# Kernel tuning notes

Hardware: AMD Instinct MI355X
Metric: run time of the kernel (lower is better)

## Reference

```python
import jax, jax.numpy as jnp
import numpy as np

H = 1024       # hidden_size
VOCAB = 32000  # output_size
L = 128        # max_length
B = 64         # batch


def setup_inputs() -> dict:
    key = jax.random.key(0)
    ks = jax.random.split(key, 16)
    inp = {
        "input_ids": jax.random.randint(ks[0], (1, B), 0, VOCAB),
        "hidden": jax.random.normal(ks[1], (1, B, H), jnp.float32),
        "encoder_outputs": jax.random.normal(ks[2], (L, B, H), jnp.float32),
        # parameters
        "emb": jax.random.normal(ks[3], (VOCAB, H), jnp.float32) * 0.02,
        "attn_W": jax.random.normal(ks[4], (H, 2 * H), jnp.float32) * 0.02,
        "attn_b": jnp.zeros((H,), jnp.float32),
        "v": jax.random.uniform(ks[5], (H,), jnp.float32),
        "w_ih": jax.random.normal(ks[6], (3 * H, 2 * H), jnp.float32) * 0.02,
        "w_hh": jax.random.normal(ks[7], (3 * H, H), jnp.float32) * 0.02,
        "b_ih": jnp.zeros((3 * H,), jnp.float32),
        "b_hh": jnp.zeros((3 * H,), jnp.float32),
        "out_W": jax.random.normal(ks[8], (VOCAB, 3 * H), jnp.float32) * 0.02,
        "out_b": jnp.zeros((VOCAB,), jnp.float32),
    }
    return inp


def reference(input_ids, hidden, encoder_outputs, emb, attn_W, attn_b, v,
              w_ih, w_hh, b_ih, b_hh, out_W, out_b):
    # Dropout in eval mode (identity).
    embedded = emb[input_ids]                      # [1, B, H]
    eo = jnp.transpose(encoder_outputs, (1, 0, 2))  # [B, L, H]
    h0 = hidden[0]                                  # [B, H]

    # Additive (Bahdanau) attention score
    h_rep = jnp.broadcast_to(h0[:, None, :], (eo.shape[0], eo.shape[1], h0.shape[-1]))
    cat = jnp.concatenate([eo, h_rep], axis=-1)     # [B, L, 2H]
    energy = jnp.tanh(jnp.einsum('blk,hk->blh', cat, attn_W) + attn_b)  # [B, L, H]
    scores = jnp.einsum('blh,h->bl', energy, v)     # [B, L]
    attention = jax.nn.softmax(scores, axis=-1)     # [B, L]
    weighted = jnp.einsum('bl,blh->bh', attention, eo)  # [B, H]

    # GRU cell (single layer, single timestep), PyTorch gate order r,z,n
    x = jnp.concatenate([embedded[0], weighted], axis=-1)  # [B, 2H]
    gx = x @ w_ih.T + b_ih                                  # [B, 3H]
    gh = h0 @ w_hh.T + b_hh                                 # [B, 3H]
    xr, xz, xn = jnp.split(gx, 3, axis=-1)
    hr, hz, hn = jnp.split(gh, 3, axis=-1)
    r = jax.nn.sigmoid(xr + hr)
    z = jax.nn.sigmoid(xz + hz)
    n = jnp.tanh(xn + r * hn)
    h_new = (1.0 - z) * n + z * h0                          # [B, H]

    out_cat = jnp.concatenate([h_new, weighted, embedded[0]], axis=-1)  # [B, 3H]
    output = out_cat @ out_W.T + out_b                      # [B, VOCAB]
    return output, h_new[None], attention[:, None, :]
```

## Files before the change

### kernel.cpp

```cpp
#include <hip/hip_runtime.h>
#include <math.h>

#define Hdim 1024
#define VOC 32000
#define LSEQ 128
#define BSZ 64

typedef __attribute__((ext_vector_type(8))) short bf16x8;
typedef __attribute__((ext_vector_type(4))) float f32x4;

__device__ __forceinline__ float fast_tanhf(float x) {
    return 1.0f - 2.0f / (__expf(2.0f * x) + 1.0f);
}
__device__ __forceinline__ float sigmoidf(float x) {
    return 1.0f / (1.0f + __expf(-x));
}
__device__ __forceinline__ short f2bf(float f) {
    unsigned u = __float_as_uint(f);
    unsigned r = (u + 0x7fffu + ((u >> 16) & 1u)) >> 16;
    return (short)r;
}

__device__ __forceinline__ void gl_lds16(const short* g, short* l) {
    __builtin_amdgcn_global_load_lds(
        (const __attribute__((address_space(1))) unsigned*)g,
        (__attribute__((address_space(3))) unsigned*)l, 16, 0, 0);
}

__device__ __forceinline__ void stage16(const float* __restrict__ src, short* dst) {
    f32x4 v0 = *(const f32x4*)(src);
    f32x4 v1 = *(const f32x4*)(src + 4);
    f32x4 v2 = *(const f32x4*)(src + 8);
    f32x4 v3 = *(const f32x4*)(src + 12);
    bf16x8 p0, p1;
    p0[0] = f2bf(v0[0]); p0[1] = f2bf(v0[1]); p0[2] = f2bf(v0[2]); p0[3] = f2bf(v0[3]);
    p0[4] = f2bf(v1[0]); p0[5] = f2bf(v1[1]); p0[6] = f2bf(v1[2]); p0[7] = f2bf(v1[3]);
    p1[0] = f2bf(v2[0]); p1[1] = f2bf(v2[1]); p1[2] = f2bf(v2[2]); p1[3] = f2bf(v2[3]);
    p1[4] = f2bf(v3[0]); p1[5] = f2bf(v3[1]); p1[6] = f2bf(v3[2]); p1[7] = f2bf(v3[3]);
    *(bf16x8*)(dst) = p0;
    *(bf16x8*)(dst + 8) = p1;
}

__global__ __launch_bounds__(256) void convert_bf16(
    const float* __restrict__ enc, const float* __restrict__ attnW,
    const float* __restrict__ hidden,
    short* __restrict__ enc_bf, short* __restrict__ attnW_bf,
    short* __restrict__ hidden_bf)
{
    const int NG_ENC = (LSEQ * BSZ * Hdim) / 8;
    const int NG_AW  = (Hdim * 2 * Hdim) / 8;
    const int NG_H   = (BSZ * Hdim) / 8;
    const int total = NG_ENC + NG_AW + NG_H;
    for (int g = blockIdx.x * 256 + threadIdx.x; g < total; g += gridDim.x * 256) {
        const float* src; short* dst; int idx;
        if (g < NG_ENC)              { src = enc;    dst = enc_bf;    idx = g; }
        else if (g < NG_ENC + NG_AW) { src = attnW;  dst = attnW_bf;  idx = g - NG_ENC; }
        else                         { src = hidden; dst = hidden_bf; idx = g - NG_ENC - NG_AW; }
        f32x4 a = *(const f32x4*)(src + (size_t)idx * 8);
        f32x4 b = *(const f32x4*)(src + (size_t)idx * 8 + 4);
        bf16x8 p;
        p[0] = f2bf(a[0]); p[1] = f2bf(a[1]); p[2] = f2bf(a[2]); p[3] = f2bf(a[3]);
        p[4] = f2bf(b[0]); p[5] = f2bf(b[1]); p[6] = f2bf(b[2]); p[7] = f2bf(b[3]);
        *(bf16x8*)(dst + (size_t)idx * 8) = p;
    }
}

__global__ __launch_bounds__(256) void ugemm(
    const short* __restrict__ A,
    const short* __restrict__ B,
    float* __restrict__ C)
{
    __shared__ short As[64 * 72];
    __shared__ short Bs[128 * 72];

    const int t = threadIdx.x;
    const int lane = t & 63, wave = t >> 6;
    const int lr = lane & 15, kh = lane >> 4;
    const int n0 = blockIdx.x * 128;
    const int kstart = blockIdx.y * 256;
    float* Cp = C + (size_t)blockIdx.y * (BSZ * Hdim);

    const int ar = t >> 2, ac = (t & 3) * 16;
    const int br = t >> 1, bc = (t & 1) * 32;

    f32x4 acc[4][2] = {};

    for (int k0 = 0; k0 < 256; k0 += 64) {
        const int kg = kstart + k0;
        {
            const short* s = A + (size_t)ar * Hdim + kg + ac;
            *(bf16x8*)(As + ar * 72 + ac)     = *(const bf16x8*)(s);
            *(bf16x8*)(As + ar * 72 + ac + 8) = *(const bf16x8*)(s + 8);
        }
        {
            const short* s = B + (size_t)(n0 + br) * (2 * Hdim) + kg + bc;
            short* d = Bs + br * 72 + bc;
            *(bf16x8*)(d)      = *(const bf16x8*)(s);
            *(bf16x8*)(d + 8)  = *(const bf16x8*)(s + 8);
            *(bf16x8*)(d + 16) = *(const bf16x8*)(s + 16);
            *(bf16x8*)(d + 24) = *(const bf16x8*)(s + 24);
        }
        __syncthreads();
#pragma unroll
        for (int kk = 0; kk < 64; kk += 32) {
            bf16x8 af[4], bfr[2];
#pragma unroll
            for (int mi = 0; mi < 4; ++mi)
                af[mi] = *(const bf16x8*)(As + (mi * 16 + lr) * 72 + kk + kh * 8);
#pragma unroll
            for (int ni = 0; ni < 2; ++ni)
                bfr[ni] = *(const bf16x8*)(Bs + (wave * 32 + ni * 16 + lr) * 72 + kk + kh * 8);
#pragma unroll
            for (int mi = 0; mi < 4; ++mi)
#pragma unroll
                for (int ni = 0; ni < 2; ++ni)
                    acc[mi][ni] = __builtin_amdgcn_mfma_f32_16x16x32_bf16(
                        af[mi], bfr[ni], acc[mi][ni], 0, 0, 0);
        }
        __syncthreads();
    }

#pragma unroll
    for (int mi = 0; mi < 4; ++mi)
#pragma unroll
        for (int ni = 0; ni < 2; ++ni) {
            const int col = n0 + wave * 32 + ni * 16 + lr;
#pragma unroll
            for (int r = 0; r < 4; ++r) {
                const int row = mi * 16 + kh * 4 + r;
                Cp[(size_t)row * Hdim + col] = acc[mi][ni][r];
            }
        }
}

__global__ __launch_bounds__(512) void attn_scores_mfma(
    const short* __restrict__ enc_bf,
    const short* __restrict__ W1_bf,
    const float* __restrict__ u4,
    const float* __restrict__ attnb,
    const float* __restrict__ vvec,
    float* __restrict__ scores_part)
{
    __shared__ short As[128 * 64];
    __shared__ short Bs[128 * 64];
    __shared__ float red[8][64];
    __shared__ float u_lds[64 * 128];

    const int t = threadIdx.x;
    const int lane = t & 63, wave = t >> 6;
    const int wr = wave >> 2, wc = wave & 3;
    const int lr = lane & 15, kh = lane >> 4;
    const int m0 = blockIdx.x * 128;
    const int n0 = blockIdx.y * 128;

    const int o1 = t * 16;
    const int o2 = 8192 + t * 16;
    const int r1 = o1 >> 7, c1 = (o1 & 127) >> 1;
    const int r2 = o2 >> 7, c2 = (o2 & 127) >> 1;

    for (int i = t; i < 64 * 128; i += 512) {
        const int b = i >> 7, hl = i & 127;
        const size_t g = (size_t)b * Hdim + n0 + hl;
        u_lds[i] = u4[g] + u4[65536 + g] + u4[2 * 65536 + g] + u4[3 * 65536 + g]
                 + attnb[n0 + hl];
    }

    f32x4 acc[4][2] = {};

    for (int kg = 0; kg < Hdim; kg += 64) {
        gl_lds16(enc_bf + (size_t)(m0 + r1) * Hdim + kg + c1, As + (o1 >> 1));
        gl_lds16(enc_bf + (size_t)(m0 + r2) * Hdim + kg + c2, As + (o2 >> 1));
        gl_lds16(W1_bf + (size_t)(n0 + r1) * (2 * Hdim) + kg + c1, Bs + (o1 >> 1));
        gl_lds16(W1_bf + (size_t)(n0 + r2) * (2 * Hdim) + kg + c2, Bs + (o2 >> 1));
        __syncthreads();
#pragma unroll
        for (int kk = 0; kk < 64; kk += 32) {
            bf16x8 af[4], bfr[2];
#pragma unroll
            for (int mi = 0; mi < 4; ++mi)
                af[mi] = *(const bf16x8*)(As + (wr * 64 + mi * 16 + lr) * 64 + kk + kh * 8);
#pragma unroll
            for (int ni = 0; ni < 2; ++ni)
                bfr[ni] = *(const bf16x8*)(Bs + (wc * 32 + ni * 16 + lr) * 64 + kk + kh * 8);
#pragma unroll
            for (int mi = 0; mi < 4; ++mi)
#pragma unroll
                for (int ni = 0; ni < 2; ++ni)
                    acc[mi][ni] = __builtin_amdgcn_mfma_f32_16x16x32_bf16(
                        af[mi], bfr[ni], acc[mi][ni], 0, 0, 0);
        }
        __syncthreads();
    }

    float sv[16];
#pragma unroll
    for (int mi = 0; mi < 4; ++mi)
#pragma unroll
        for (int r = 0; r < 4; ++r) {
            const int lrow = mi * 16 + kh * 4 + r;
            const int b = lrow;
            float s = 0.0f;
#pragma unroll
            for (int ni = 0; ni < 2; ++ni) {
                const int hl = wc * 32 + ni * 16 + lr;
                const float e = fast_tanhf(acc[mi][ni][r] + u_lds[b * 128 + hl]);
                s += e * vvec[n0 + hl];
            }
            sv[mi * 4 + r] = s;
        }
#pragma unroll
    for (int i = 0; i < 16; ++i) {
#pragma unroll
        for (int d = 1; d < 16; d <<= 1)
            sv[i] += __shfl_xor(sv[i], d, 64);
    }
    if (lr == 0) {
#pragma unroll
        for (int mi = 0; mi < 4; ++mi)
#pragma unroll
            for (int r = 0; r < 4; ++r)
                red[wave][mi * 16 + kh * 4 + r] = sv[mi * 4 + r];
    }
    __syncthreads();
    if (t < 128) {
        const int wrr = t >> 6, lrow = t & 63;
        scores_part[(size_t)blockIdx.y * (LSEQ * BSZ) + m0 + t] =
            red[wrr * 4 + 0][lrow] + red[wrr * 4 + 1][lrow] +
            red[wrr * 4 + 2][lrow] + red[wrr * 4 + 3][lrow];
    }
}

__global__ __launch_bounds__(128) void softmax_weighted(
    const float* __restrict__ sp,
    const short* __restrict__ enc_bf,
    const int* __restrict__ ids,
    const float* __restrict__ emb,
    float* __restrict__ attn_out,
    short* __restrict__ x_bf,
    short* __restrict__ oc_bf)
{
    const int b = blockIdx.x, hg = blockIdx.y, t = threadIdx.x;
    __shared__ float aw[LSEQ];
    __shared__ float red[LSEQ];

    if (hg == 0) {
        const int id = ids[b];
        const int h = t * 8;
        f32x4 e0 = *(const f32x4*)(emb + (size_t)id * Hdim + h);
        f32x4 e1 = *(const f32x4*)(emb + (size_t)id * Hdim + h + 4);
        bf16x8 p;
        p[0] = f2bf(e0[0]); p[1] = f2bf(e0[1]); p[2] = f2bf(e0[2]); p[3] = f2bf(e0[3]);
        p[4] = f2bf(e1[0]); p[5] = f2bf(e1[1]); p[6] = f2bf(e1[2]); p[7] = f2bf(e1[3]);
        *(bf16x8*)(x_bf + (size_t)b * 2048 + h) = p;
        *(bf16x8*)(oc_bf + (size_t)b * 3072 + 2048 + h) = p;
    }

    float s = 0.0f;
#pragma unroll
    for (int g = 0; g < 8; ++g) s += sp[g * (LSEQ * BSZ) + t * 64 + b];
    red[t] = s;
    __syncthreads();
    for (int off = 64; off > 0; off >>= 1) {
        if (t < off) red[t] = fmaxf(red[t], red[t + off]);
        __syncthreads();
    }
    const float mx = red[0];
    __syncthreads();
    const float e = __expf(s - mx);
    red[t] = e;
    __syncthreads();
    for (int off = 64; off > 0; off >>= 1) {
        if (t < off) red[t] += red[t + off];
        __syncthreads();
    }
    const float p = e / red[0];
    aw[t] = p;
    if (hg == 0) attn_out[(size_t)b * LSEQ + t] = p;
    __syncthreads();

    const int h = hg * 256 + t * 2;
    float a0 = 0.0f, a1 = 0.0f;
#pragma unroll 8
    for (int l = 0; l < LSEQ; ++l) {
        const unsigned w = *(const unsigned*)(enc_bf + ((size_t)l * BSZ + b) * Hdim + h);
        const float pw = aw[l];
        a0 = fmaf(pw, __uint_as_float(w << 16), a0);
        a1 = fmaf(pw, __uint_as_float(w & 0xffff0000u), a1);
    }
    const unsigned packed = (unsigned)(unsigned short)f2bf(a0)
                          | ((unsigned)(unsigned short)f2bf(a1) << 16);
    *(unsigned*)(x_bf + (size_t)b * 2048 + 1024 + h) = packed;
    *(unsigned*)(oc_bf + (size_t)b * 3072 + 1024 + h) = packed;
}

__device__ __forceinline__ void sgemm_body(
    const short* __restrict__ A, int lda,
    const float* __restrict__ B, int ldb,
    const float* __restrict__ bias,
    float* __restrict__ C, int ldc,
    int n0, int kstart, int klen)
{
    __shared__ short As[2][64 * 72];
    __shared__ short Bs[2][64 * 72];

    const int t = threadIdx.x;
    const int lane = t & 63, wave = t >> 6;
    const int wm = wave >> 2, wn = wave & 3;
    const int lr = lane & 15, kh = lane >> 4;

    const int sr = t >> 3, sc = (t & 7) * 8;
    const short* Ap = A + (size_t)sr * lda + kstart + sc;
    const float* Bp = B + (size_t)(n0 + sr) * ldb + kstart + sc;

    const int nkt = klen >> 6;

    bf16x8 pa = *(const bf16x8*)(Ap);
    f32x4 pb0 = *(const f32x4*)(Bp);
    f32x4 pb1 = *(const f32x4*)(Bp + 4);
    *(bf16x8*)(&As[0][sr * 72 + sc]) = pa;
    {
        bf16x8 q;
        q[0] = f2bf(pb0[0]); q[1] = f2bf(pb0[1]); q[2] = f2bf(pb0[2]); q[3] = f2bf(pb0[3]);
        q[4] = f2bf(pb1[0]); q[5] = f2bf(pb1[1]); q[6] = f2bf(pb1[2]); q[7] = f2bf(pb1[3]);
        *(bf16x8*)(&Bs[0][sr * 72 + sc]) = q;
    }

    f32x4 acc[2] = {};

    for (int kt = 0; kt < nkt; ++kt) {
        const int cur = kt & 1;
        if (kt + 1 < nkt) {
            const int kn = (kt + 1) * 64;
            pa  = *(const bf16x8*)(Ap + kn);
            pb0 = *(const f32x4*)(Bp + kn);
            pb1 = *(const f32x4*)(Bp + kn + 4);
        }
        __syncthreads();
#pragma unroll
        for (int kk = 0; kk < 64; kk += 32) {
            bf16x8 af0 = *(const bf16x8*)(&As[cur][(wm * 32 + lr) * 72 + kk + kh * 8]);
            bf16x8 af1 = *(const bf16x8*)(&As[cur][(wm * 32 + 16 + lr) * 72 + kk + kh * 8]);
            bf16x8 bfr = *(const bf16x8*)(&Bs[cur][(wn * 16 + lr) * 72 + kk + kh * 8]);
            acc[0] = __builtin_amdgcn_mfma_f32_16x16x32_bf16(af0, bfr, acc[0], 0, 0, 0);
            acc[1] = __builtin_amdgcn_mfma_f32_16x16x32_bf16(af1, bfr, acc[1], 0, 0, 0);
        }
        if (kt + 1 < nkt) {
            const int nxt = cur ^ 1;
            *(bf16x8*)(&As[nxt][sr * 72 + sc]) = pa;
            bf16x8 q;
            q[0] = f2bf(pb0[0]); q[1] = f2bf(pb0[1]); q[2] = f2bf(pb0[2]); q[3] = f2bf(pb0[3]);
            q[4] = f2bf(pb1[0]); q[5] = f2bf(pb1[1]); q[6] = f2bf(pb1[2]); q[7] = f2bf(pb1[3]);
            *(bf16x8*)(&Bs[nxt][sr * 72 + sc]) = q;
        }
    }

    const int col = n0 + wn * 16 + lr;
    const float bb = bias ? bias[col] : 0.0f;
#pragma unroll
    for (int mi = 0; mi < 2; ++mi)
#pragma unroll
        for (int r = 0; r < 4; ++r) {
            const int row = wm * 32 + mi * 16 + kh * 4 + r;
            C[(size_t)row * ldc + col] = acc[mi][r] + bb;
        }
}

__global__ __launch_bounds__(512) void outproj_stream(
    const short* __restrict__ A, const float* __restrict__ B,
    const float* __restrict__ bias, float* __restrict__ logits)
{
    sgemm_body(A, 3 * Hdim, B, 3 * Hdim, bias, logits, VOC,
               blockIdx.x * 64, 0, 3 * Hdim);
}

__global__ __launch_bounds__(512) void gxgh_stream(
    const short* __restrict__ x_bf, const float* __restrict__ w_ih,
    const short* __restrict__ hidden_bf, const float* __restrict__ w_hh,
    float* __restrict__ gx4, float* __restrict__ gh4)
{
    const size_t P = (size_t)BSZ * 3 * Hdim;
    if (blockIdx.x < 48)
        sgemm_body(x_bf, 2 * Hdim, w_ih, 2 * Hdim, nullptr,
                   gx4 + blockIdx.y * P, 3 * Hdim,
                   blockIdx.x * 64, blockIdx.y * 512, 512);
    else
        sgemm_body(hidden_bf, Hdim, w_hh, Hdim, nullptr,
                   gh4 + blockIdx.y * P, 3 * Hdim,
                   (blockIdx.x - 48) * 64, blockIdx.y * 256, 256);
}

__global__ __launch_bounds__(256) void gru_kernel(
    const float* __restrict__ gx4, const float* __restrict__ gh4,
    const float* __restrict__ b_ih, const float* __restrict__ b_hh,
    const float* __restrict__ h0,
    float* __restrict__ hnew_out, short* __restrict__ oc_bf)
{
    const int idx = blockIdx.x * 256 + threadIdx.x;
    const int b = idx >> 10, h = idx & 1023;
    const size_t g3 = (size_t)b * (3 * Hdim);
    const size_t P = (size_t)BSZ * 3 * Hdim;
    float xr = b_ih[h], xz = b_ih[Hdim + h], xn = b_ih[2 * Hdim + h];
    float hr = b_hh[h], hz = b_hh[Hdim + h], hn = b_hh[2 * Hdim + h];
#pragma unroll
    for (int s = 0; s < 4; ++s) {
        xr += gx4[s * P + g3 + h];
        xz += gx4[s * P + g3 + Hdim + h];
        xn += gx4[s * P + g3 + 2 * Hdim + h];
        hr += gh4[s * P + g3 + h];
        hz += gh4[s * P + g3 + Hdim + h];
        hn += gh4[s * P + g3 + 2 * Hdim + h];
    }
    const float r = sigmoidf(xr + hr);
    const float z = sigmoidf(xz + hz);
    const float n = fast_tanhf(xn + r * hn);
    const float hv = (1.0f - z) * n + z * h0[(size_t)b * Hdim + h];
    hnew_out[(size_t)b * Hdim + h] = hv;
    oc_bf[g3 + h] = f2bf(hv);
}

extern "C" void kernel_launch(void* const* d_in, const int* in_sizes, int n_in,
                              void* d_out, int out_size, void* d_ws, size_t ws_size,
                              hipStream_t stream)
{
    const int*   ids    = (const int*)d_in[0];
    const float* hidden = (const float*)d_in[1];
    const float* enc    = (const float*)d_in[2];
    const float* emb    = (const float*)d_in[3];
    const float* attnW  = (const float*)d_in[4];
    const float* attnb  = (const float*)d_in[5];
    const float* vvec   = (const float*)d_in[6];
    const float* w_ih   = (const float*)d_in[7];
    const float* w_hh   = (const float*)d_in[8];
    const float* b_ih   = (const float*)d_in[9];
    const float* b_hh   = (const float*)d_in[10];
    const float* out_W  = (const float*)d_in[11];
    const float* out_b  = (const float*)d_in[12];

    float* out        = (float*)d_out;
    float* out_logits = out;
    float* out_hnew   = out + (size_t)BSZ * VOC;
    float* out_attn   = out_hnew + (size_t)BSZ * Hdim;

    float* ws = (float*)d_ws;
    short* enc_bf    = (short*)ws;
    short* attnW_bf  = (short*)(ws + 4194304);
    short* hidden_bf = (short*)(ws + 5242880);
    float* ws_u4  = ws + 5275648;
    float* ws_sp  = ws_u4 + 262144;
    short* x_bf   = (short*)(ws_sp + 65536);
    short* oc_bf  = (short*)(ws_sp + 131072);
    float* ws_gx4 = ws_sp + 229376;
    float* ws_gh4 = ws_gx4 + 786432;

    convert_bf16<<<dim3(1024), 256, 0, stream>>>(
        enc, attnW, hidden, enc_bf, attnW_bf, hidden_bf);

    ugemm<<<dim3(Hdim / 128, 4), 256, 0, stream>>>(
        hidden_bf, attnW_bf + Hdim, ws_u4);

    attn_scores_mfma<<<dim3(LSEQ / 2, 8), 512, 0, stream>>>(
        enc_bf, attnW_bf, ws_u4, attnb, vvec, ws_sp);

    softmax_weighted<<<dim3(BSZ, 4), 128, 0, stream>>>(
        ws_sp, enc_bf, ids, emb, out_attn, x_bf, oc_bf);

    gxgh_stream<<<dim3(96, 4), 512, 0, stream>>>(
        x_bf, w_ih, hidden_bf, w_hh, ws_gx4, ws_gh4);

    gru_kernel<<<dim3(BSZ * Hdim / 256), 256, 0, stream>>>(
        ws_gx4, ws_gh4, b_ih, b_hh, hidden, out_hnew, oc_bf);

    outproj_stream<<<dim3(VOC / 64), 512, 0, stream>>>(
        oc_bf, out_W, out_b, out_logits);
}
```

Before: 174.1 us.

## Split output projection and overlap embedding part with attention GEMM

The output projection is split by K. The embedding slice of out_W, which only needs the embedding, now runs in the same launch as the attention-score GEMM, with blocks interleaved. The remaining h_new/weighted slice runs last and accumulates into the logits. The bf16 conversion and the hidden·W2 u-GEMM are fused into one launch that also gathers the embedding, and only the needed half of attn_W is converted. This removes launches and fills idle CUs during the attention phase, at the cost of a second read-modify-write pass over the logits and more complex block dispatch.

```diff
diff --git a/kernel.cpp b/kernel.cpp
--- a/kernel.cpp
+++ b/kernel.cpp
@@ -41,45 +41,54 @@
     *(bf16x8*)(dst + 8) = p1;
 }
 
-__global__ __launch_bounds__(256) void convert_bf16(
+__global__ __launch_bounds__(256) void conv_ug(
     const float* __restrict__ enc, const float* __restrict__ attnW,
-    const float* __restrict__ hidden,
-    short* __restrict__ enc_bf, short* __restrict__ attnW_bf,
-    short* __restrict__ hidden_bf)
-{
-    const int NG_ENC = (LSEQ * BSZ * Hdim) / 8;
-    const int NG_AW  = (Hdim * 2 * Hdim) / 8;
-    const int NG_H   = (BSZ * Hdim) / 8;
-    const int total = NG_ENC + NG_AW + NG_H;
-    for (int g = blockIdx.x * 256 + threadIdx.x; g < total; g += gridDim.x * 256) {
-        const float* src; short* dst; int idx;
-        if (g < NG_ENC)              { src = enc;    dst = enc_bf;    idx = g; }
-        else if (g < NG_ENC + NG_AW) { src = attnW;  dst = attnW_bf;  idx = g - NG_ENC; }
-        else                         { src = hidden; dst = hidden_bf; idx = g - NG_ENC - NG_AW; }
-        f32x4 a = *(const f32x4*)(src + (size_t)idx * 8);
-        f32x4 b = *(const f32x4*)(src + (size_t)idx * 8 + 4);
-        bf16x8 p;
-        p[0] = f2bf(a[0]); p[1] = f2bf(a[1]); p[2] = f2bf(a[2]); p[3] = f2bf(a[3]);
-        p[4] = f2bf(b[0]); p[5] = f2bf(b[1]); p[6] = f2bf(b[2]); p[7] = f2bf(b[3]);
-        *(bf16x8*)(dst + (size_t)idx * 8) = p;
-    }
-}
-
-__global__ __launch_bounds__(256) void ugemm(
-    const short* __restrict__ A,
-    const short* __restrict__ B,
-    float* __restrict__ C)
+    const float* __restrict__ hidden, const float* __restrict__ emb,
+    const int* __restrict__ ids,
+    short* __restrict__ enc_bf, short* __restrict__ attnW1_bf,
+    short* __restrict__ hidden_bf, short* __restrict__ x_bf,
+    float* __restrict__ u4)
 {
     __shared__ short As[64 * 72];
     __shared__ short Bs[128 * 72];
+
+    if (blockIdx.x < 1024) {
+        const int NG_ENC = 1048576, NG_AW = 131072, NG_H = 8192, NG_EMB = 8192;
+        const int total = NG_ENC + NG_AW + NG_H + NG_EMB;
+        for (int g = blockIdx.x * 256 + threadIdx.x; g < total; g += 1024 * 256) {
+            const float* src; short* dst;
+            if (g < NG_ENC) {
+                src = enc + (size_t)g * 8; dst = enc_bf + (size_t)g * 8;
+            } else if (g < NG_ENC + NG_AW) {
+                const int i = g - NG_ENC, h = i >> 7, c = i & 127;
+                src = attnW + (size_t)h * 2048 + c * 8;
+                dst = attnW1_bf + (size_t)h * 1024 + c * 8;
+            } else if (g < NG_ENC + NG_AW + NG_H) {
+                const int i = g - NG_ENC - NG_AW;
+                src = hidden + (size_t)i * 8; dst = hidden_bf + (size_t)i * 8;
+            } else {
+                const int i = g - NG_ENC - NG_AW - NG_H, b = i >> 7, c = i & 127;
+                src = emb + (size_t)ids[b] * Hdim + c * 8;
+                dst = x_bf + (size_t)b * 2048 + c * 8;
+            }
+            f32x4 a = *(const f32x4*)(src);
+            f32x4 b = *(const f32x4*)(src + 4);
+            bf16x8 p;
+            p[0] = f2bf(a[0]); p[1] = f2bf(a[1]); p[2] = f2bf(a[2]); p[3] = f2bf(a[3]);
+            p[4] = f2bf(b[0]); p[5] = f2bf(b[1]); p[6] = f2bf(b[2]); p[7] = f2bf(b[3]);
+            *(bf16x8*)(dst) = p;
+        }
+        return;
+    }
+
+    const int id = blockIdx.x - 1024;
+    const int n0 = (id & 7) * 128;
+    const int kstart = (id >> 3) * 256;
+    float* Cp = u4 + (size_t)(id >> 3) * (BSZ * Hdim);
 
     const int t = threadIdx.x;
     const int lane = t & 63, wave = t >> 6;
     const int lr = lane & 15, kh = lane >> 4;
-    const int n0 = blockIdx.x * 128;
-    const int kstart = blockIdx.y * 256;
-    float* Cp = C + (size_t)blockIdx.y * (BSZ * Hdim);
-
     const int ar = t >> 2, ac = (t & 3) * 16;
     const int br = t >> 1, bc = (t & 1) * 32;
 
@@ -87,19 +96,9 @@
 
     for (int k0 = 0; k0 < 256; k0 += 64) {
         const int kg = kstart + k0;
-        {
-            const short* s = A + (size_t)ar * Hdim + kg + ac;
-            *(bf16x8*)(As + ar * 72 + ac)     = *(const bf16x8*)(s);
-            *(bf16x8*)(As + ar * 72 + ac + 8) = *(const bf16x8*)(s + 8);
-        }
-        {
-            const short* s = B + (size_t)(n0 + br) * (2 * Hdim) + kg + bc;
-            short* d = Bs + br * 72 + bc;
-            *(bf16x8*)(d)      = *(const bf16x8*)(s);
-            *(bf16x8*)(d + 8)  = *(const bf16x8*)(s + 8);
-            *(bf16x8*)(d + 16) = *(const bf16x8*)(s + 16);
-            *(bf16x8*)(d + 24) = *(const bf16x8*)(s + 24);
-        }
+        stage16(hidden + (size_t)ar * Hdim + kg + ac, As + ar * 72 + ac);
+        stage16(attnW + (size_t)(n0 + br) * 2048 + 1024 + kg + bc,      Bs + br * 72 + bc);
+        stage16(attnW + (size_t)(n0 + br) * 2048 + 1024 + kg + bc + 16, Bs + br * 72 + bc + 16);
         __syncthreads();
 #pragma unroll
         for (int kk = 0; kk < 64; kk += 32) {
@@ -126,79 +125,150 @@
         for (int ni = 0; ni < 2; ++ni) {
             const int col = n0 + wave * 32 + ni * 16 + lr;
 #pragma unroll
-            for (int r = 0; r < 4; ++r) {
-                const int row = mi * 16 + kh * 4 + r;
-                Cp[(size_t)row * Hdim + col] = acc[mi][ni][r];
-            }
-        }
-}
-
-__global__ __launch_bounds__(512) void attn_scores_mfma(
-    const short* __restrict__ enc_bf,
-    const short* __restrict__ W1_bf,
-    const float* __restrict__ u4,
-    const float* __restrict__ attnb,
-    const float* __restrict__ vvec,
-    float* __restrict__ scores_part)
-{
-    __shared__ short As[128 * 64];
-    __shared__ short Bs[128 * 64];
-    __shared__ float red[8][64];
-    __shared__ float u_lds[64 * 128];
+            for (int r = 0; r < 4; ++r)
+                Cp[(size_t)(mi * 16 + kh * 4 + r) * Hdim + col] = acc[mi][ni][r];
+        }
+}
+
+__device__ __forceinline__ void sgemm_body(
+    char* smem,
+    const short* __restrict__ A, int lda,
+    const float* __restrict__ B, int ldb,
+    const float* __restrict__ bias,
+    float* __restrict__ C, int ldc,
+    int n0, int kstart, int klen, bool rmw)
+{
+    short* As = (short*)smem;
+    short* Bs = (short*)(smem + 18432);
+
+    const int t = threadIdx.x;
+    const int lane = t & 63, wave = t >> 6;
+    const int wm = wave >> 2, wn = wave & 3;
+    const int lr = lane & 15, kh = lane >> 4;
+
+    const int sr = t >> 3, sc = (t & 7) * 8;
+    const short* Ap = A + (size_t)sr * lda + kstart + sc;
+    const float* Bp = B + (size_t)(n0 + sr) * ldb + kstart + sc;
+
+    const int nkt = klen >> 6;
+
+    bf16x8 pa = *(const bf16x8*)(Ap);
+    f32x4 pb0 = *(const f32x4*)(Bp);
+    f32x4 pb1 = *(const f32x4*)(Bp + 4);
+    *(bf16x8*)(&As[sr * 72 + sc]) = pa;
+    {
+        bf16x8 q;
+        q[0] = f2bf(pb0[0]); q[1] = f2bf(pb0[1]); q[2] = f2bf(pb0[2]); q[3] = f2bf(pb0[3]);
+        q[4] = f2bf(pb1[0]); q[5] = f2bf(pb1[1]); q[6] = f2bf(pb1[2]); q[7] = f2bf(pb1[3]);
+        *(bf16x8*)(&Bs[sr * 72 + sc]) = q;
+    }
+
+    f32x4 acc[2] = {};
+
+    for (int kt = 0; kt < nkt; ++kt) {
+        const int co = (kt & 1) * 4608;
+        if (kt + 1 < nkt) {
+            const int kn = (kt + 1) * 64;
+            pa  = *(const bf16x8*)(Ap + kn);
+            pb0 = *(const f32x4*)(Bp + kn);
+            pb1 = *(const f32x4*)(Bp + kn + 4);
+        }
+        __syncthreads();
+#pragma unroll
+        for (int kk = 0; kk < 64; kk += 32) {
+            bf16x8 af0 = *(const bf16x8*)(&As[co + (wm * 32 + lr) * 72 + kk + kh * 8]);
+            bf16x8 af1 = *(const bf16x8*)(&As[co + (wm * 32 + 16 + lr) * 72 + kk + kh * 8]);
+            bf16x8 bfr = *(const bf16x8*)(&Bs[co + (wn * 16 + lr) * 72 + kk + kh * 8]);
+            acc[0] = __builtin_amdgcn_mfma_f32_16x16x32_bf16(af0, bfr, acc[0], 0, 0, 0);
+            acc[1] = __builtin_amdgcn_mfma_f32_16x16x32_bf16(af1, bfr, acc[1], 0, 0, 0);
+        }
+        if (kt + 1 < nkt) {
+            const int no = ((kt + 1) & 1) * 4608;
+            *(bf16x8*)(&As[no + sr * 72 + sc]) = pa;
+            bf16x8 q;
+            q[0] = f2bf(pb0[0]); q[1] = f2bf(pb0[1]); q[2] = f2bf(pb0[2]); q[3] = f2bf(pb0[3]);
+            q[4] = f2bf(pb1[0]); q[5] = f2bf(pb1[1]); q[6] = f2bf(pb1[2]); q[7] = f2bf(pb1[3]);
+            *(bf16x8*)(&Bs[no + sr * 72 + sc]) = q;
+        }
+    }
+
+    const int col = n0 + wn * 16 + lr;
+    const float bb = bias ? bias[col] : 0.0f;
+#pragma unroll
+    for (int mi = 0; mi < 2; ++mi)
+#pragma unroll
+        for (int r = 0; r < 4; ++r) {
+            const size_t idx = (size_t)(wm * 32 + mi * 16 + kh * 4 + r) * ldc + col;
+            const float prev = rmw ? C[idx] : 0.0f;
+            C[idx] = prev + acc[mi][r] + bb;
+        }
+}
+
+__device__ __forceinline__ void attn_body(
+    char* smem,
+    const short* __restrict__ enc_bf, const short* __restrict__ W1_bf,
+    const float* __restrict__ u4, const float* __restrict__ attnb,
+    const float* __restrict__ vvec, float* __restrict__ scores_part,
+    int aid)
+{
+    short* As = (short*)smem;
+    short* Bs = (short*)(smem + 16384);
+    float* red = (float*)(smem + 32768);
 
     const int t = threadIdx.x;
     const int lane = t & 63, wave = t >> 6;
     const int wr = wave >> 2, wc = wave & 3;
     const int lr = lane & 15, kh = lane >> 4;
-    const int m0 = blockIdx.x * 128;
-    const int n0 = blockIdx.y * 128;
+    const int m0 = (aid & 63) * 128;
+    const int n0 = (aid >> 6) * 128;
 
     const int o1 = t * 16;
     const int o2 = 8192 + t * 16;
     const int r1 = o1 >> 7, c1 = (o1 & 127) >> 1;
     const int r2 = o2 >> 7, c2 = (o2 & 127) >> 1;
 
+    f32x4 acc[4][2] = {};
+
+    for (int kg = 0; kg < Hdim; kg += 64) {
+        gl_lds16(enc_bf + (size_t)(m0 + r1) * Hdim + kg + c1, As + (o1 >> 1));
+        gl_lds16(enc_bf + (size_t)(m0 + r2) * Hdim + kg + c2, As + (o2 >> 1));
+        gl_lds16(W1_bf + (size_t)(n0 + r1) * Hdim + kg + c1, Bs + (o1 >> 1));
+        gl_lds16(W1_bf + (size_t)(n0 + r2) * Hdim + kg + c2, Bs + (o2 >> 1));
+        __syncthreads();
+#pragma unroll
+        for (int kk = 0; kk < 64; kk += 32) {
+            bf16x8 af[4], bfr[2];
+#pragma unroll
+            for (int mi = 0; mi < 4; ++mi)
+                af[mi] = *(const bf16x8*)(As + (wr * 64 + mi * 16 + lr) * 64 + kk + kh * 8);
+#pragma unroll
+            for (int ni = 0; ni < 2; ++ni)
+                bfr[ni] = *(const bf16x8*)(Bs + (wc * 32 + ni * 16 + lr) * 64 + kk + kh * 8);
+#pragma unroll
+            for (int mi = 0; mi < 4; ++mi)
+#pragma unroll
+                for (int ni = 0; ni < 2; ++ni)
+                    acc[mi][ni] = __builtin_amdgcn_mfma_f32_16x16x32_bf16(
+                        af[mi], bfr[ni], acc[mi][ni], 0, 0, 0);
+        }
+        __syncthreads();
+    }
+
+    float* u_lds = (float*)smem;
     for (int i = t; i < 64 * 128; i += 512) {
         const int b = i >> 7, hl = i & 127;
         const size_t g = (size_t)b * Hdim + n0 + hl;
         u_lds[i] = u4[g] + u4[65536 + g] + u4[2 * 65536 + g] + u4[3 * 65536 + g]
                  + attnb[n0 + hl];
     }
-
-    f32x4 acc[4][2] = {};
-
-    for (int kg = 0; kg < Hdim; kg += 64) {
-        gl_lds16(enc_bf + (size_t)(m0 + r1) * Hdim + kg + c1, As + (o1 >> 1));
-        gl_lds16(enc_bf + (size_t)(m0 + r2) * Hdim + kg + c2, As + (o2 >> 1));
-        gl_lds16(W1_bf + (size_t)(n0 + r1) * (2 * Hdim) + kg + c1, Bs + (o1 >> 1));
-        gl_lds16(W1_bf + (size_t)(n0 + r2) * (2 * Hdim) + kg + c2, Bs + (o2 >> 1));
-        __syncthreads();
-#pragma unroll
-        for (int kk = 0; kk < 64; kk += 32) {
-            bf16x8 af[4], bfr[2];
-#pragma unroll
-            for (int mi = 0; mi < 4; ++mi)
-                af[mi] = *(const bf16x8*)(As + (wr * 64 + mi * 16 + lr) * 64 + kk + kh * 8);
-#pragma unroll
-            for (int ni = 0; ni < 2; ++ni)
-                bfr[ni] = *(const bf16x8*)(Bs + (wc * 32 + ni * 16 + lr) * 64 + kk + kh * 8);
-#pragma unroll
-            for (int mi = 0; mi < 4; ++mi)
-#pragma unroll
-                for (int ni = 0; ni < 2; ++ni)
-                    acc[mi][ni] = __builtin_amdgcn_mfma_f32_16x16x32_bf16(
-                        af[mi], bfr[ni], acc[mi][ni], 0, 0, 0);
-        }
-        __syncthreads();
-    }
+    __syncthreads();
 
     float sv[16];
 #pragma unroll
     for (int mi = 0; mi < 4; ++mi)
 #pragma unroll
         for (int r = 0; r < 4; ++r) {
-            const int lrow = mi * 16 + kh * 4 + r;
-            const int b = lrow;
+            const int b = mi * 16 + kh * 4 + r;
             float s = 0.0f;
 #pragma unroll
             for (int ni = 0; ni < 2; ++ni) {
@@ -219,41 +289,48 @@
         for (int mi = 0; mi < 4; ++mi)
 #pragma unroll
             for (int r = 0; r < 4; ++r)
-                red[wave][mi * 16 + kh * 4 + r] = sv[mi * 4 + r];
+                red[wave * 64 + mi * 16 + kh * 4 + r] = sv[mi * 4 + r];
     }
     __syncthreads();
     if (t < 128) {
         const int wrr = t >> 6, lrow = t & 63;
-        scores_part[(size_t)blockIdx.y * (LSEQ * BSZ) + m0 + t] =
-            red[wrr * 4 + 0][lrow] + red[wrr * 4 + 1][lrow] +
-            red[wrr * 4 + 2][lrow] + red[wrr * 4 + 3][lrow];
+        scores_part[(size_t)(aid >> 6) * (LSEQ * BSZ) + m0 + t] =
+            red[(wrr * 4 + 0) * 64 + lrow] + red[(wrr * 4 + 1) * 64 + lrow] +
+            red[(wrr * 4 + 2) * 64 + lrow] + red[(wrr * 4 + 3) * 64 + lrow];
+    }
+}
+
+__global__ __launch_bounds__(512) void attn_oproj(
+    const short* __restrict__ enc_bf, const short* __restrict__ W1_bf,
+    const float* __restrict__ u4, const float* __restrict__ attnb,
+    const float* __restrict__ vvec, float* __restrict__ scores_part,
+    const short* __restrict__ x_bf, const float* __restrict__ out_W,
+    const float* __restrict__ out_b, float* __restrict__ logits)
+{
+    __shared__ __align__(16) char smem[36864];
+    const int i = blockIdx.x;
+    if (i < 1000) {
+        if ((i & 1) == 0)
+            attn_body(smem, enc_bf, W1_bf, u4, attnb, vvec, scores_part, i >> 1);
+        else
+            sgemm_body(smem, x_bf, 2048, out_W + 2048, 3072, out_b,
+                       logits, VOC, (i >> 1) * 64, 0, 1024, false);
+    } else {
+        attn_body(smem, enc_bf, W1_bf, u4, attnb, vvec, scores_part,
+                  500 + (i - 1000));
     }
 }
 
 __global__ __launch_bounds__(128) void softmax_weighted(
     const float* __restrict__ sp,
     const short* __restrict__ enc_bf,
-    const int* __restrict__ ids,
-    const float* __restrict__ emb,
     float* __restrict__ attn_out,
     short* __restrict__ x_bf,
-    short* __restrict__ oc_bf)
+    short* __restrict__ hw_bf)
 {
     const int b = blockIdx.x, hg = blockIdx.y, t = threadIdx.x;
     __shared__ float aw[LSEQ];
     __shared__ float red[LSEQ];
-
-    if (hg == 0) {
-        const int id = ids[b];
-        const int h = t * 8;
-        f32x4 e0 = *(const f32x4*)(emb + (size_t)id * Hdim + h);
-        f32x4 e1 = *(const f32x4*)(emb + (size_t)id * Hdim + h + 4);
-        bf16x8 p;
-        p[0] = f2bf(e0[0]); p[1] = f2bf(e0[1]); p[2] = f2bf(e0[2]); p[3] = f2bf(e0[3]);
-        p[4] = f2bf(e1[0]); p[5] = f2bf(e1[1]); p[6] = f2bf(e1[2]); p[7] = f2bf(e1[3]);
-        *(bf16x8*)(x_bf + (size_t)b * 2048 + h) = p;
-        *(bf16x8*)(oc_bf + (size_t)b * 3072 + 2048 + h) = p;
-    }
 
     float s = 0.0f;
 #pragma unroll
@@ -290,87 +367,7 @@
     const unsigned packed = (unsigned)(unsigned short)f2bf(a0)
                           | ((unsigned)(unsigned short)f2bf(a1) << 16);
     *(unsigned*)(x_bf + (size_t)b * 2048 + 1024 + h) = packed;
-    *(unsigned*)(oc_bf + (size_t)b * 3072 + 1024 + h) = packed;
-}
-
-__device__ __forceinline__ void sgemm_body(
-    const short* __restrict__ A, int lda,
-    const float* __restrict__ B, int ldb,
-    const float* __restrict__ bias,
-    float* __restrict__ C, int ldc,
-    int n0, int kstart, int klen)
-{
-    __shared__ short As[2][64 * 72];
-    __shared__ short Bs[2][64 * 72];
-
-    const int t = threadIdx.x;
-    const int lane = t & 63, wave = t >> 6;
-    const int wm = wave >> 2, wn = wave & 3;
-    const int lr = lane & 15, kh = lane >> 4;
-
-    const int sr = t >> 3, sc = (t & 7) * 8;
-    const short* Ap = A + (size_t)sr * lda + kstart + sc;
-    const float* Bp = B + (size_t)(n0 + sr) * ldb + kstart + sc;
-
-    const int nkt = klen >> 6;
-
-    bf16x8 pa = *(const bf16x8*)(Ap);
-    f32x4 pb0 = *(const f32x4*)(Bp);
-    f32x4 pb1 = *(const f32x4*)(Bp + 4);
-    *(bf16x8*)(&As[0][sr * 72 + sc]) = pa;
-    {
-        bf16x8 q;
-        q[0] = f2bf(pb0[0]); q[1] = f2bf(pb0[1]); q[2] = f2bf(pb0[2]); q[3] = f2bf(pb0[3]);
-        q[4] = f2bf(pb1[0]); q[5] = f2bf(pb1[1]); q[6] = f2bf(pb1[2]); q[7] = f2bf(pb1[3]);
-        *(bf16x8*)(&Bs[0][sr * 72 + sc]) = q;
-    }
-
-    f32x4 acc[2] = {};
-
-    for (int kt = 0; kt < nkt; ++kt) {
-        const int cur = kt & 1;
-        if (kt + 1 < nkt) {
-            const int kn = (kt + 1) * 64;
-            pa  = *(const bf16x8*)(Ap + kn);
-            pb0 = *(const f32x4*)(Bp + kn);
-            pb1 = *(const f32x4*)(Bp + kn + 4);
-        }
-        __syncthreads();
-#pragma unroll
-        for (int kk = 0; kk < 64; kk += 32) {
-            bf16x8 af0 = *(const bf16x8*)(&As[cur][(wm * 32 + lr) * 72 + kk + kh * 8]);
-            bf16x8 af1 = *(const bf16x8*)(&As[cur][(wm * 32 + 16 + lr) * 72 + kk + kh * 8]);
-            bf16x8 bfr = *(const bf16x8*)(&Bs[cur][(wn * 16 + lr) * 72 + kk + kh * 8]);
-            acc[0] = __builtin_amdgcn_mfma_f32_16x16x32_bf16(af0, bfr, acc[0], 0, 0, 0);
-            acc[1] = __builtin_amdgcn_mfma_f32_16x16x32_bf16(af1, bfr, acc[1], 0, 0, 0);
-        }
-        if (kt + 1 < nkt) {
-            const int nxt = cur ^ 1;
-            *(bf16x8*)(&As[nxt][sr * 72 + sc]) = pa;
-            bf16x8 q;
-            q[0] = f2bf(pb0[0]); q[1] = f2bf(pb0[1]); q[2] = f2bf(pb0[2]); q[3] = f2bf(pb0[3]);
-            q[4] = f2bf(pb1[0]); q[5] = f2bf(pb1[1]); q[6] = f2bf(pb1[2]); q[7] = f2bf(pb1[3]);
-            *(bf16x8*)(&Bs[nxt][sr * 72 + sc]) = q;
-        }
-    }
-
-    const int col = n0 + wn * 16 + lr;
-    const float bb = bias ? bias[col] : 0.0f;
-#pragma unroll
-    for (int mi = 0; mi < 2; ++mi)
-#pragma unroll
-        for (int r = 0; r < 4; ++r) {
-            const int row = wm * 32 + mi * 16 + kh * 4 + r;
-            C[(size_t)row * ldc + col] = acc[mi][r] + bb;
-        }
-}
-
-__global__ __launch_bounds__(512) void outproj_stream(
-    const short* __restrict__ A, const float* __restrict__ B,
-    const float* __restrict__ bias, float* __restrict__ logits)
-{
-    sgemm_body(A, 3 * Hdim, B, 3 * Hdim, bias, logits, VOC,
-               blockIdx.x * 64, 0, 3 * Hdim);
+    *(unsigned*)(hw_bf + (size_t)b * 2048 + 1024 + h) = packed;
 }
 
 __global__ __launch_bounds__(512) void gxgh_stream(
@@ -378,22 +375,23 @@
     const short* __restrict__ hidden_bf, const float* __restrict__ w_hh,
     float* __restrict__ gx4, float* __restrict__ gh4)
 {
+    __shared__ __align__(16) char smem[36864];
     const size_t P = (size_t)BSZ * 3 * Hdim;
     if (blockIdx.x < 48)
-        sgemm_body(x_bf, 2 * Hdim, w_ih, 2 * Hdim, nullptr,
+        sgemm_body(smem, x_bf, 2 * Hdim, w_ih, 2 * Hdim, nullptr,
                    gx4 + blockIdx.y * P, 3 * Hdim,
-                   blockIdx.x * 64, blockIdx.y * 512, 512);
+                   blockIdx.x * 64, blockIdx.y * 512, 512, false);
     else
-        sgemm_body(hidden_bf, Hdim, w_hh, Hdim, nullptr,
+        sgemm_body(smem, hidden_bf, Hdim, w_hh, Hdim, nullptr,
                    gh4 + blockIdx.y * P, 3 * Hdim,
-                   (blockIdx.x - 48) * 64, blockIdx.y * 256, 256);
+                   (blockIdx.x - 48) * 64, blockIdx.y * 256, 256, false);
 }
 
 __global__ __launch_bounds__(256) void gru_kernel(
     const float* __restrict__ gx4, const float* __restrict__ gh4,
     const float* __restrict__ b_ih, const float* __restrict__ b_hh,
     const float* __restrict__ h0,
-    float* __restrict__ hnew_out, short* __restrict__ oc_bf)
+    float* __restrict__ hnew_out, short* __restrict__ hw_bf)
 {
     const int idx = blockIdx.x * 256 + threadIdx.x;
     const int b = idx >> 10, h = idx & 1023;
@@ -415,7 +413,16 @@
     const float n = fast_tanhf(xn + r * hn);
     const float hv = (1.0f - z) * n + z * h0[(size_t)b * Hdim + h];
     hnew_out[(size_t)b * Hdim + h] = hv;
-    oc_bf[g3 + h] = f2bf(hv);
+    hw_bf[(size_t)b * 2048 + h] = f2bf(hv);
+}
+
+__global__ __launch_bounds__(512) void oproj_hw(
+    const short* __restrict__ hw_bf, const float* __restrict__ out_W,
+    float* __restrict__ logits)
+{
+    __shared__ __align__(16) char smem[36864];
+    sgemm_body(smem, hw_bf, 2048, out_W, 3072, nullptr,
+               logits, VOC, blockIdx.x * 64, 0, 2048, true);
 }
 
 extern "C" void kernel_launch(void* const* d_in, const int* in_sizes, int n_in,
@@ -443,33 +450,32 @@
 
     float* ws = (float*)d_ws;
     short* enc_bf    = (short*)ws;
-    short* attnW_bf  = (short*)(ws + 4194304);
-    short* hidden_bf = (short*)(ws + 5242880);
-    float* ws_u4  = ws + 5275648;
-    float* ws_sp  = ws_u4 + 262144;
-    short* x_bf   = (short*)(ws_sp + 65536);
-    short* oc_bf  = (short*)(ws_sp + 131072);
-    float* ws_gx4 = ws_sp + 229376;
-    float* ws_gh4 = ws_gx4 + 786432;
-
-    convert_bf16<<<dim3(1024), 256, 0, stream>>>(
-        enc, attnW, hidden, enc_bf, attnW_bf, hidden_bf);
-
-    ugemm<<<dim3(Hdim / 128, 4), 256, 0, stream>>>(
-        hidden_bf, attnW_bf + Hdim, ws_u4);
-
-    attn_scores_mfma<<<dim3(LSEQ / 2, 8), 512, 0, stream>>>(
-        enc_bf, attnW_bf, ws_u4, attnb, vvec, ws_sp);
+    short* attnW1_bf = (short*)(ws + 4194304);
+    short* hidden_bf = (short*)(ws + 4718592);
+    float* ws_u4     = ws + 4751360;
+    float* ws_sp     = ws_u4 + 262144;
+    short* x_bf      = (short*)(ws_sp + 65536);
+    short* hw_bf     = (short*)(ws_sp + 131072);
+    float* ws_gx4    = ws_sp + 196608;
+    float* ws_gh4    = ws_gx4 + 786432;
+
+    conv_ug<<<dim3(1056), 256, 0, stream>>>(
+        enc, attnW, hidden, emb, ids,
+        enc_bf, attnW1_bf, hidden_bf, x_bf, ws_u4);
+
+    attn_oproj<<<dim3(1012), 512, 0, stream>>>(
+        enc_bf, attnW1_bf, ws_u4, attnb, vvec, ws_sp,
+        x_bf, out_W, out_b, out_logits);
 
     softmax_weighted<<<dim3(BSZ, 4), 128, 0, stream>>>(
-        ws_sp, enc_bf, ids, emb, out_attn, x_bf, oc_bf);
+        ws_sp, enc_bf, out_attn, x_bf, hw_bf);
 
     gxgh_stream<<<dim3(96, 4), 512, 0, stream>>>(
         x_bf, w_ih, hidden_bf, w_hh, ws_gx4, ws_gh4);
 
     gru_kernel<<<dim3(BSZ * Hdim / 256), 256, 0, stream>>>(
-        ws_gx4, ws_gh4, b_ih, b_hh, hidden, out_hnew, oc_bf);
-
-    outproj_stream<<<dim3(VOC / 64), 512, 0, stream>>>(
-        oc_bf, out_W, out_b, out_logits);
-}
+        ws_gx4, ws_gh4, b_ih, b_hh, hidden, out_hnew, hw_bf);
+
+    oproj_hw<<<dim3(VOC / 64), 512, 0, stream>>>(
+        hw_bf, out_W, out_logits);
+}
```

Measured after the change: 177.1 us. About the same (+1.7%).
